# Kernel tuning notes

Hardware: AMD Instinct MI355X
Metric: run time of the kernel (lower is better)

## Reference

```python
import jax, jax.numpy as jnp
import numpy as np

ATTWSIZE = 64  # sliding window length (matches init_kwargs attwsize)


def setup_inputs() -> dict:
    key = jax.random.key(0)
    k1, k2, k3 = jax.random.split(key, 3)
    B, T, D, A = 32, 4096, 256, 128
    x = jax.random.normal(k1, (B, T, D), dtype=jnp.float32)
    Wp = jax.random.normal(k2, (A, D), dtype=jnp.float32) / np.sqrt(D).astype(np.float32)
    bp = jnp.zeros((A,), dtype=jnp.float32)
    Wg = jax.random.normal(k3, (1, A), dtype=jnp.float32) / np.sqrt(A).astype(np.float32)
    return {"x": x, "Wp": Wp, "bp": bp, "Wg": Wg}


def _windowed_sum(v, w):
    # causal sliding-window sum over axis=1: sum(v[:, max(t-w+1,0):t+1, :])
    # single-pass cumsum formulation: cs[t] - cs[t-w]
    cs = jnp.cumsum(v, axis=1)
    T = v.shape[1]
    shifted = jnp.pad(cs, ((0, 0), (w, 0), (0, 0)))[:, :T, :]
    return cs - shifted


def reference(x, Wp, bp, Wg):
    # proj = tanh(Linear(dimio->dimatt)(x))
    proj = jnp.tanh(jnp.einsum('btd,ad->bta', x, Wp) + bp)
    # gvec = sigmoid(Linear(dimatt->1, no bias)(proj))  -> [B, T, 1]
    g = jax.nn.sigmoid(jnp.einsum('bta,oa->bto', proj, Wg))
    wx = g * x  # gated input [B, T, D]
    num = _windowed_sum(wx, ATTWSIZE)         # [B, T, D]
    den = _windowed_sum(g, ATTWSIZE)          # [B, T, 1] broadcasts over D
    return num / den
```

## Files before the change

### kernel.cpp

```cpp
#include <hip/hip_runtime.h>

#define TT 4096
#define DD 256
#define AA 128
#define WIN 64

typedef short bf16x8 __attribute__((ext_vector_type(8)));
typedef float f32x4 __attribute__((ext_vector_type(4)));

__device__ __forceinline__ unsigned short f2bf(float f) {
    unsigned int u = __builtin_bit_cast(unsigned int, f);
    u += 0x7FFFu + ((u >> 16) & 1u);
    return (unsigned short)(u >> 16);
}

__global__ __launch_bounds__(256) void prep_wp(const float* __restrict__ Wp,
                                               unsigned short* __restrict__ wpb) {
    int i = blockIdx.x * 256 + threadIdx.x;
    wpb[i] = f2bf(Wp[i]);
}

#define LDK 264
#define RTILE 128
#define NSUB 2

__global__ __launch_bounds__(256, 3) void gate_kernel(
        const float* __restrict__ x, const unsigned short* __restrict__ wpb,
        const float* __restrict__ bp, const float* __restrict__ Wg,
        float* __restrict__ g) {
    __shared__ unsigned short xs[64 * LDK];
    __shared__ float psum[4][64];
    const int tid  = threadIdx.x;
    const int lane = tid & 63;
    const int wave = tid >> 6;
    const int quad = lane >> 4;
    const int nrow = lane & 15;
    const long row0 = (long)blockIdx.x * RTILE;

    bf16x8 bfrag[2][8];
    float bpv[2], wgv[2];
#pragma unroll
    for (int nt = 0; nt < 2; ++nt) {
        int n = wave * 32 + nt * 16 + nrow;
        bpv[nt] = bp[n];
        wgv[nt] = Wg[n];
#pragma unroll
        for (int k0 = 0; k0 < 8; ++k0)
            bfrag[nt][k0] = *reinterpret_cast<const bf16x8*>(
                wpb + n * DD + k0 * 32 + quad * 8);
    }

    for (int s = 0; s < NSUB; ++s) {
        const float* xsrc = x + (row0 + s * 64) * DD;
#pragma unroll
        for (int it = 0; it < 16; ++it) {
            int idx = it * 256 + tid;
            int r   = idx >> 6;
            int c4  = idx & 63;
            float4 v = reinterpret_cast<const float4*>(xsrc + r * DD)[c4];
            ushort4 h;
            h.x = f2bf(v.x); h.y = f2bf(v.y); h.z = f2bf(v.z); h.w = f2bf(v.w);
            *reinterpret_cast<ushort4*>(&xs[r * LDK + c4 * 4]) = h;
        }
        __syncthreads();

        f32x4 acc[4][2];
#pragma unroll
        for (int mt = 0; mt < 4; ++mt)
#pragma unroll
            for (int nt = 0; nt < 2; ++nt)
                acc[mt][nt] = (f32x4){0.f, 0.f, 0.f, 0.f};

#pragma unroll
        for (int k0 = 0; k0 < 8; ++k0) {
#pragma unroll
            for (int mt = 0; mt < 4; ++mt) {
                bf16x8 af = *reinterpret_cast<const bf16x8*>(
                    &xs[(mt * 16 + nrow) * LDK + quad * 8 + k0 * 32]);
                acc[mt][0] = __builtin_amdgcn_mfma_f32_16x16x32_bf16(af, bfrag[0][k0], acc[mt][0], 0, 0, 0);
                acc[mt][1] = __builtin_amdgcn_mfma_f32_16x16x32_bf16(af, bfrag[1][k0], acc[mt][1], 0, 0, 0);
            }
        }

        float p[4][4];
#pragma unroll
        for (int mt = 0; mt < 4; ++mt)
#pragma unroll
            for (int r = 0; r < 4; ++r) p[mt][r] = 0.f;
#pragma unroll
        for (int nt = 0; nt < 2; ++nt) {
#pragma unroll
            for (int mt = 0; mt < 4; ++mt) {
#pragma unroll
                for (int r = 0; r < 4; ++r) {
                    float pre = acc[mt][nt][r] + bpv[nt];
                    float e  = __expf(2.0f * pre);
                    float th = 1.0f - 2.0f * __builtin_amdgcn_rcpf(e + 1.0f);
                    p[mt][r] += th * wgv[nt];
                }
            }
        }
#pragma unroll
        for (int off = 1; off <= 8; off <<= 1)
#pragma unroll
            for (int mt = 0; mt < 4; ++mt)
#pragma unroll
                for (int r = 0; r < 4; ++r)
                    p[mt][r] += __shfl_xor(p[mt][r], off, 64);
        if (nrow == 0) {
#pragma unroll
            for (int mt = 0; mt < 4; ++mt)
#pragma unroll
                for (int r = 0; r < 4; ++r)
                    psum[wave][mt * 16 + quad * 4 + r] = p[mt][r];
        }
        __syncthreads();
        if (tid < 64) {
            float ssum = psum[0][tid] + psum[1][tid] + psum[2][tid] + psum[3][tid];
            g[row0 + s * 64 + tid] = __builtin_amdgcn_rcpf(1.0f + __expf(-ssum));
        }
        __syncthreads();
    }
}

#define TC 128
#define NCHUNK (TT / TC)

__global__ __launch_bounds__(256) void stream_kernel(
        const float* __restrict__ x, const float* __restrict__ g,
        float* __restrict__ out) {
    __shared__ float gbuf[TC + WIN];
    const int b     = blockIdx.x >> 5;
    const int chunk = blockIdx.x & (NCHUNK - 1);
    const int t0    = chunk * TC;
    const int d     = threadIdx.x;
    const float* xb = x + (size_t)b * TT * DD;
    const float* gb = g + (size_t)b * TT;
    float* ob = out + (size_t)b * TT * DD;

    if (d < TC + WIN) {
        int s = t0 - WIN + d;
        gbuf[d] = (s >= 0) ? gb[s] : 0.f;
    }
    __syncthreads();

    float S = 0.f, Sg = 0.f;
#pragma unroll 16
    for (int i = 0; i < WIN; ++i) {
        int s  = t0 - WIN + i;
        int sc = s < 0 ? 0 : s;
        float gv = gbuf[i];
        S  += gv * xb[(size_t)sc * DD + d];
        Sg += gv;
    }

#pragma unroll 8
    for (int tt = 0; tt < TC; ++tt) {
        int t  = t0 + tt;
        int ts = t - WIN;
        int tsc = ts < 0 ? 0 : ts;
        float gnew = gbuf[WIN + tt];
        float gold = gbuf[tt];
        float vnew = gnew * xb[(size_t)t * DD + d];
        float vold = gold * xb[(size_t)tsc * DD + d];
        S  += vnew - vold;
        Sg += gnew - gold;
        ob[(size_t)t * DD + d] = S * __builtin_amdgcn_rcpf(Sg);
    }
}

extern "C" void kernel_launch(void* const* d_in, const int* in_sizes, int n_in,
                              void* d_out, int out_size, void* d_ws, size_t ws_size,
                              hipStream_t stream) {
    const float* x  = (const float*)d_in[0];
    const float* Wp = (const float*)d_in[1];
    const float* bp = (const float*)d_in[2];
    const float* Wg = (const float*)d_in[3];
    float* out = (float*)d_out;

    unsigned short* wpb = (unsigned short*)d_ws;
    float* g = (float*)((char*)d_ws + 65536);

    prep_wp<<<AA * DD / 256, 256, 0, stream>>>(Wp, wpb);
    gate_kernel<<<32 * TT / RTILE, 256, 0, stream>>>(x, wpb, bp, Wg, g);
    stream_kernel<<<32 * NCHUNK, 256, 0, stream>>>(x, g, out);
}
```

Measured before the change: 310.7 us.

## Load gate-kernel A fragments directly from global memory and enlarge stream chunks

The gate kernel no longer stages x through shared memory as bf16. Each wave now loads its own row fragments straight from global memory, converts them in registers and feeds the MFMAs, which removes the LDS round trip and one barrier. Every wave reads the full 64-row tile, so each wave issues redundant global loads (about 4x per block) and relies on the caches to absorb them. Separately, the stream kernel's time chunk grows from 128 to 256, halving the warm-up window reads per output row at the cost of fewer blocks.

Result: no change. 310.7 us (+0.0%).

```diff
diff --git a/kernel.cpp b/kernel.cpp
--- a/kernel.cpp
+++ b/kernel.cpp
@@ -20,22 +20,19 @@
     wpb[i] = f2bf(Wp[i]);
 }
 
-#define LDK 264
-#define RTILE 128
-#define NSUB 2
+#define RPB 64
 
-__global__ __launch_bounds__(256, 3) void gate_kernel(
+__global__ __launch_bounds__(256) void gate_kernel(
         const float* __restrict__ x, const unsigned short* __restrict__ wpb,
         const float* __restrict__ bp, const float* __restrict__ Wg,
         float* __restrict__ g) {
-    __shared__ unsigned short xs[64 * LDK];
-    __shared__ float psum[4][64];
+    __shared__ float psum[4][RPB];
     const int tid  = threadIdx.x;
     const int lane = tid & 63;
     const int wave = tid >> 6;
     const int quad = lane >> 4;
     const int nrow = lane & 15;
-    const long row0 = (long)blockIdx.x * RTILE;
+    const long row0 = (long)blockIdx.x * RPB;
 
     bf16x8 bfrag[2][8];
     float bpv[2], wgv[2];
@@ -50,87 +47,81 @@
                 wpb + n * DD + k0 * 32 + quad * 8);
     }
 
-    for (int s = 0; s < NSUB; ++s) {
-        const float* xsrc = x + (row0 + s * 64) * DD;
+    f32x4 acc[4][2];
 #pragma unroll
-        for (int it = 0; it < 16; ++it) {
-            int idx = it * 256 + tid;
-            int r   = idx >> 6;
-            int c4  = idx & 63;
-            float4 v = reinterpret_cast<const float4*>(xsrc + r * DD)[c4];
-            ushort4 h;
-            h.x = f2bf(v.x); h.y = f2bf(v.y); h.z = f2bf(v.z); h.w = f2bf(v.w);
-            *reinterpret_cast<ushort4*>(&xs[r * LDK + c4 * 4]) = h;
+    for (int mt = 0; mt < 4; ++mt)
+#pragma unroll
+        for (int nt = 0; nt < 2; ++nt)
+            acc[mt][nt] = (f32x4){0.f, 0.f, 0.f, 0.f};
+
+#pragma unroll
+    for (int mt = 0; mt < 4; ++mt) {
+        const float* xrow = x + (row0 + mt * 16 + nrow) * DD + quad * 8;
+        float4 xa[8][2];
+#pragma unroll
+        for (int k0 = 0; k0 < 8; ++k0) {
+            xa[k0][0] = *reinterpret_cast<const float4*>(xrow + k0 * 32);
+            xa[k0][1] = *reinterpret_cast<const float4*>(xrow + k0 * 32 + 4);
         }
-        __syncthreads();
+#pragma unroll
+        for (int k0 = 0; k0 < 8; ++k0) {
+            bf16x8 af;
+            af[0] = (short)f2bf(xa[k0][0].x); af[1] = (short)f2bf(xa[k0][0].y);
+            af[2] = (short)f2bf(xa[k0][0].z); af[3] = (short)f2bf(xa[k0][0].w);
+            af[4] = (short)f2bf(xa[k0][1].x); af[5] = (short)f2bf(xa[k0][1].y);
+            af[6] = (short)f2bf(xa[k0][1].z); af[7] = (short)f2bf(xa[k0][1].w);
+            acc[mt][0] = __builtin_amdgcn_mfma_f32_16x16x32_bf16(af, bfrag[0][k0], acc[mt][0], 0, 0, 0);
+            acc[mt][1] = __builtin_amdgcn_mfma_f32_16x16x32_bf16(af, bfrag[1][k0], acc[mt][1], 0, 0, 0);
+        }
+    }
 
-        f32x4 acc[4][2];
+    float p[4][4];
+#pragma unroll
+    for (int mt = 0; mt < 4; ++mt)
+#pragma unroll
+        for (int r = 0; r < 4; ++r) p[mt][r] = 0.f;
+#pragma unroll
+    for (int nt = 0; nt < 2; ++nt) {
+#pragma unroll
+        for (int mt = 0; mt < 4; ++mt) {
+#pragma unroll
+            for (int r = 0; r < 4; ++r) {
+                float pre = acc[mt][nt][r] + bpv[nt];
+                float e  = __expf(2.0f * pre);
+                float th = 1.0f - 2.0f * __builtin_amdgcn_rcpf(e + 1.0f);
+                p[mt][r] += th * wgv[nt];
+            }
+        }
+    }
+#pragma unroll
+    for (int off = 1; off <= 8; off <<= 1)
 #pragma unroll
         for (int mt = 0; mt < 4; ++mt)
 #pragma unroll
-            for (int nt = 0; nt < 2; ++nt)
-                acc[mt][nt] = (f32x4){0.f, 0.f, 0.f, 0.f};
-
-#pragma unroll
-        for (int k0 = 0; k0 < 8; ++k0) {
-#pragma unroll
-            for (int mt = 0; mt < 4; ++mt) {
-                bf16x8 af = *reinterpret_cast<const bf16x8*>(
-                    &xs[(mt * 16 + nrow) * LDK + quad * 8 + k0 * 32]);
-                acc[mt][0] = __builtin_amdgcn_mfma_f32_16x16x32_bf16(af, bfrag[0][k0], acc[mt][0], 0, 0, 0);
-                acc[mt][1] = __builtin_amdgcn_mfma_f32_16x16x32_bf16(af, bfrag[1][k0], acc[mt][1], 0, 0, 0);
-            }
-        }
-
-        float p[4][4];
+            for (int r = 0; r < 4; ++r)
+                p[mt][r] += __shfl_xor(p[mt][r], off, 64);
+    if (nrow == 0) {
 #pragma unroll
         for (int mt = 0; mt < 4; ++mt)
 #pragma unroll
-            for (int r = 0; r < 4; ++r) p[mt][r] = 0.f;
-#pragma unroll
-        for (int nt = 0; nt < 2; ++nt) {
-#pragma unroll
-            for (int mt = 0; mt < 4; ++mt) {
-#pragma unroll
-                for (int r = 0; r < 4; ++r) {
-                    float pre = acc[mt][nt][r] + bpv[nt];
-                    float e  = __expf(2.0f * pre);
-                    float th = 1.0f - 2.0f * __builtin_amdgcn_rcpf(e + 1.0f);
-                    p[mt][r] += th * wgv[nt];
-                }
-            }
-        }
-#pragma unroll
-        for (int off = 1; off <= 8; off <<= 1)
-#pragma unroll
-            for (int mt = 0; mt < 4; ++mt)
-#pragma unroll
-                for (int r = 0; r < 4; ++r)
-                    p[mt][r] += __shfl_xor(p[mt][r], off, 64);
-        if (nrow == 0) {
-#pragma unroll
-            for (int mt = 0; mt < 4; ++mt)
-#pragma unroll
-                for (int r = 0; r < 4; ++r)
-                    psum[wave][mt * 16 + quad * 4 + r] = p[mt][r];
-        }
-        __syncthreads();
-        if (tid < 64) {
-            float ssum = psum[0][tid] + psum[1][tid] + psum[2][tid] + psum[3][tid];
-            g[row0 + s * 64 + tid] = __builtin_amdgcn_rcpf(1.0f + __expf(-ssum));
-        }
-        __syncthreads();
+            for (int r = 0; r < 4; ++r)
+                psum[wave][mt * 16 + quad * 4 + r] = p[mt][r];
+    }
+    __syncthreads();
+    if (tid < RPB) {
+        float ssum = psum[0][tid] + psum[1][tid] + psum[2][tid] + psum[3][tid];
+        g[row0 + tid] = __builtin_amdgcn_rcpf(1.0f + __expf(-ssum));
     }
 }
 
-#define TC 128
+#define TC 256
 #define NCHUNK (TT / TC)
 
 __global__ __launch_bounds__(256) void stream_kernel(
         const float* __restrict__ x, const float* __restrict__ g,
         float* __restrict__ out) {
     __shared__ float gbuf[TC + WIN];
-    const int b     = blockIdx.x >> 5;
+    const int b     = blockIdx.x >> 4;
     const int chunk = blockIdx.x & (NCHUNK - 1);
     const int t0    = chunk * TC;
     const int d     = threadIdx.x;
@@ -138,9 +129,9 @@
     const float* gb = g + (size_t)b * TT;
     float* ob = out + (size_t)b * TT * DD;
 
-    if (d < TC + WIN) {
-        int s = t0 - WIN + d;
-        gbuf[d] = (s >= 0) ? gb[s] : 0.f;
+    for (int i = d; i < TC + WIN; i += 256) {
+        int s = t0 - WIN + i;
+        gbuf[i] = (s >= 0) ? gb[s] : 0.f;
     }
     __syncthreads();
 
@@ -182,6 +173,6 @@
     float* g = (float*)((char*)d_ws + 65536);
 
     prep_wp<<<AA * DD / 256, 256, 0, stream>>>(Wp, wpb);
-    gate_kernel<<<32 * TT / RTILE, 256, 0, stream>>>(x, wpb, bp, Wg, g);
+    gate_kernel<<<32 * TT / RPB, 256, 0, stream>>>(x, wpb, bp, Wg, g);
     stream_kernel<<<32 * NCHUNK, 256, 0, stream>>>(x, g, out);
 }
```
